# Kernel tuning notes

Hardware: AMD Instinct MI355X
Metric: run time of the kernel (lower is better)

The kernel has to match this reference:

```python
import jax, jax.numpy as jnp
import numpy as np

B, DIM, HEADS, HW = 32, 384, 8, 48
CH = DIM // HEADS  # 48 channels per head


def pool_matrix(H, s):
    # PyTorch AdaptiveAvgPool2d binning: start=floor(i*H/s), end=ceil((i+1)*H/s)
    P = np.zeros((s, H), np.float32)
    for i in range(s):
        a = (i * H) // s
        b = -((-(i + 1) * H) // s)
        P[i, a:b] = 1.0 / (b - a)
    return jnp.asarray(P)


def dwconv(x, w, b, p):
    # depthwise conv, NCHW, kernel [C,1,k,k], stride 1, symmetric pad p
    y = jax.lax.conv_general_dilated(
        x, w, (1, 1), [(p, p), (p, p)],
        dimension_numbers=('NCHW', 'OIHW', 'NCHW'),
        feature_group_count=x.shape[1])
    if b is not None:
        y = y + b[None, :, None, None]
    return y


def setup_inputs() -> dict:
    key = jax.random.key(0)
    ks = jax.random.split(key, 10)
    s = 0.02
    return {
        'x': jax.random.normal(ks[0], (B, DIM, HW, HW), jnp.float32),
        'ln_w': jnp.ones((DIM,), jnp.float32),
        'ln_b': jnp.zeros((DIM,), jnp.float32),
        'w_qkv': jax.random.normal(ks[1], (3 * DIM, DIM), jnp.float32) * s,
        'w_dw': jax.random.normal(ks[2], (3 * DIM, 1, 3, 3), jnp.float32) * s,
        'temperature': jnp.ones((HEADS, 1, 1), jnp.float32),
        'conv3_w': jax.random.normal(ks[3], (3 * CH, 1, 3, 3), jnp.float32) * s,
        'conv3_b': jnp.zeros((3 * CH,), jnp.float32),
        'conv5_w': jax.random.normal(ks[4], (3 * CH, 1, 5, 5), jnp.float32) * s,
        'conv5_b': jnp.zeros((3 * CH,), jnp.float32),
        'conv7_w': jax.random.normal(ks[5], (2 * CH, 1, 7, 7), jnp.float32) * s,
        'conv7_b': jnp.zeros((2 * CH,), jnp.float32),
        'w_proj': jax.random.normal(ks[6], (DIM, DIM), jnp.float32) * s,
    }


def reference(x, ln_w, ln_b, w_qkv, w_dw, temperature,
              conv3_w, conv3_b, conv5_w, conv5_b, conv7_w, conv7_b, w_proj):
    b, C, H, W = x.shape
    heads, Ch = HEADS, C // HEADS
    N = H * W
    # WithBias LayerNorm over channel dim (biased variance, eps 1e-5)
    mu = x.mean(axis=1, keepdims=True)
    var = ((x - mu) ** 2).mean(axis=1, keepdims=True)
    xn = (x - mu) / jnp.sqrt(var + 1e-5) * ln_w[None, :, None, None] + ln_b[None, :, None, None]
    # qkv: 1x1 conv then depthwise 3x3 (groups = 3*dim)
    qkv = jnp.einsum('bchw,oc->bohw', xn, w_qkv)
    qkv = dwconv(qkv, w_dw, None, 1)
    q, k, v = jnp.split(qkv, 3, axis=1)
    q = q.reshape(b, heads, Ch, N)
    k = k.reshape(b, heads, Ch, N)
    v = v.reshape(b, heads, Ch, N)
    # L2-normalize along token dim (F.normalize eps=1e-12)
    qn = q / jnp.maximum(jnp.linalg.norm(q, axis=-1, keepdims=True), 1e-12)
    kn = k / jnp.maximum(jnp.linalg.norm(k, axis=-1, keepdims=True), 1e-12)
    # channel attention [b,h,Ch,Ch]
    attn = jax.nn.relu(jnp.einsum('bhcn,bhdn->bhcd', qn, kn) * temperature[None])
    # ---- FilterModule (crpe) ----
    v_img = v.reshape(b, heads * Ch, H, W)
    # low-pass: 4 equal channel chunks, adaptive avg pool to (1,3,5,7), bilinear up
    chunk = (heads * Ch) // 4
    lp_parts = []
    for idx, sz in enumerate((1, 3, 5, 7)):
        part = v_img[:, idx * chunk:(idx + 1) * chunk]
        Pr = pool_matrix(H, sz)
        Pc = pool_matrix(W, sz)
        pooled = jnp.einsum('ph,bchw,qw->bcpq', Pr, part, Pc)
        lp_parts.append(jax.image.resize(pooled, (b, chunk, H, W), method='linear'))
    LP = jax.nn.relu(jnp.concatenate(lp_parts, axis=1))
    # high-pass: grouped depthwise convs on [3Ch, 3Ch, 2Ch] channel splits
    s0, s1 = 3 * Ch, 3 * Ch
    HP = jnp.concatenate([
        dwconv(v_img[:, :s0], conv3_w, conv3_b, 1),
        dwconv(v_img[:, s0:s0 + s1], conv5_w, conv5_b, 2),
        dwconv(v_img[:, s0 + s1:], conv7_w, conv7_b, 3),
    ], axis=1)
    HP = HP.reshape(b, heads, Ch, N)
    LPf = LP.reshape(b, heads, Ch, N)
    crpe = qn * HP + LPf
    # ---- output ----
    out = jnp.einsum('bhcd,bhdn->bhcn', attn, v)
    out = (Ch ** -0.5) * out + crpe
    out = out.reshape(b, C, H, W)
    out = jnp.einsum('bchw,oc->bohw', out, w_proj)
    return out
```

## Files before the change

### kernel.cpp

```cpp
#include <hip/hip_runtime.h>

typedef unsigned short u16;
typedef short sh4 __attribute__((ext_vector_type(4)));
typedef short short8 __attribute__((ext_vector_type(8)));
typedef u16 ush8 __attribute__((ext_vector_type(8)));
typedef __bf16 bf16x8 __attribute__((ext_vector_type(8)));
typedef float f32x4 __attribute__((ext_vector_type(4)));

#define NB 32
#define CDIM 384
#define NSP 2304
#define QCH 1152

__device__ __forceinline__ float b2f(u16 u) {
    union { unsigned i; float f; } v; v.i = ((unsigned)u) << 16; return v.f;
}
__device__ __forceinline__ u16 f2b(float f) {
    union { float f; unsigned i; } v; v.f = f;
    unsigned r = v.i + 0x7FFFu + ((v.i >> 16) & 1u);
    return (u16)(r >> 16);
}
__device__ __forceinline__ void gload16(const u16* g, u16* l) {
    __builtin_amdgcn_global_load_lds((const __attribute__((address_space(1))) unsigned int*)(g),
                                     (__attribute__((address_space(3))) unsigned int*)(l), 16, 0, 0);
}

__global__ __launch_bounds__(256) void k_prep(const float* __restrict__ wqkv,
                                              const float* __restrict__ wproj,
                                              u16* __restrict__ wqkv_bf,
                                              u16* __restrict__ wproj_bf) {
    int i = blockIdx.x * 256 + threadIdx.x;
    if (i < QCH * CDIM) wqkv_bf[i] = f2b(wqkv[i]);
    if (i < CDIM * CDIM) wproj_bf[i] = f2b(wproj[i]);
}

__global__ __launch_bounds__(256) void k_ln(const float* __restrict__ x,
                                            const float* __restrict__ lnw,
                                            const float* __restrict__ lnb,
                                            u16* __restrict__ xnt) {
    __shared__ float s_sum[4][64], s_sq[4][64], s_mu[64], s_rs[64];
    __shared__ u16 s_tile[64][392];
    int b = blockIdx.y, n0 = blockIdx.x * 64;
    int tid = threadIdx.x, c4 = tid >> 6, nl = tid & 63;
    int cbase = c4 * 96;
    const float* xb = x + (size_t)b * CDIM * NSP + (size_t)cbase * NSP + n0 + nl;
    float v[96];
    float sum = 0.f, sq = 0.f;
#pragma unroll
    for (int j = 0; j < 96; j++) {
        v[j] = xb[(size_t)j * NSP];
        sum += v[j]; sq += v[j] * v[j];
    }
    s_sum[c4][nl] = sum; s_sq[c4][nl] = sq;
    __syncthreads();
    if (tid < 64) {
        float s = s_sum[0][tid] + s_sum[1][tid] + s_sum[2][tid] + s_sum[3][tid];
        float q = s_sq[0][tid] + s_sq[1][tid] + s_sq[2][tid] + s_sq[3][tid];
        float mu = s * (1.f / CDIM);
        float var = q * (1.f / CDIM) - mu * mu;
        s_mu[tid] = mu; s_rs[tid] = rsqrtf(var + 1e-5f);
    }
    __syncthreads();
    float mu = s_mu[nl], rs = s_rs[nl];
#pragma unroll
    for (int j = 0; j < 96; j++) {
        int c = cbase + j;
        s_tile[nl][c] = f2b((v[j] - mu) * rs * lnw[c] + lnb[c]);
    }
    __syncthreads();
    u16* o = xnt + ((size_t)b * NSP + n0) * CDIM;
    for (int i = tid; i < 64 * 48; i += 256) {
        int row = i / 48, c8 = i % 48;
        *(short8*)(o + row * CDIM + c8 * 8) = *(const short8*)(&s_tile[row][c8 * 8]);
    }
}

__global__ __launch_bounds__(256) void k_gemm(const u16* __restrict__ A,
                                              const u16* __restrict__ Bt,
                                              void* __restrict__ Cmat, int M, int f32out) {
    __shared__ __align__(16) u16 As[128 * 64];
    __shared__ __align__(16) u16 Bs[128 * 64];
    int tid = threadIdx.x;
    int bxn = blockIdx.x, bym = blockIdx.y, bz = blockIdx.z;
    int wave = tid >> 6, lane = tid & 63, wr = wave >> 1, wc = wave & 1;
    int lr = lane & 15, lk = lane >> 4;
    f32x4 acc[4][4];
#pragma unroll
    for (int m = 0; m < 4; m++)
#pragma unroll
        for (int n = 0; n < 4; n++) acc[m][n] = (f32x4){0.f, 0.f, 0.f, 0.f};
    int coloff = ((lane & 7) ^ (lane >> 3)) * 8;
    int rsub = lane >> 3;
    const u16* Ag = A + (size_t)(bym * 128 + wave * 32 + rsub) * 384 + coloff;
    const u16* Bg = Bt + ((size_t)bz * NSP + bxn * 128 + wave * 32 + rsub) * 384 + coloff;
    u16* Al = As + (wave * 4) * 512;
    u16* Bl = Bs + (wave * 4) * 512;
    for (int k0 = 0; k0 < 384; k0 += 64) {
#pragma unroll
        for (int i = 0; i < 4; i++) {
            gload16(Ag + (size_t)(i * 8) * 384 + k0, Al + i * 512);
            gload16(Bg + (size_t)(i * 8) * 384 + k0, Bl + i * 512);
        }
        __syncthreads();
        short8 bfr[4][2];
#pragma unroll
        for (int n = 0; n < 4; n++) {
            int row = wc * 64 + n * 16 + lr;
#pragma unroll
            for (int h = 0; h < 2; h++)
                bfr[n][h] = *(const short8*)(Bs + row * 64 + ((h * 4 + lk) ^ (lr & 7)) * 8);
        }
#pragma unroll
        for (int m = 0; m < 4; m++) {
            int row = wr * 64 + m * 16 + lr;
            short8 a0 = *(const short8*)(As + row * 64 + ((lk) ^ (lr & 7)) * 8);
            short8 a1 = *(const short8*)(As + row * 64 + ((4 + lk) ^ (lr & 7)) * 8);
#pragma unroll
            for (int n = 0; n < 4; n++) {
                acc[m][n] = __builtin_amdgcn_mfma_f32_16x16x32_bf16(
                    __builtin_bit_cast(bf16x8, a0), __builtin_bit_cast(bf16x8, bfr[n][0]),
                    acc[m][n], 0, 0, 0);
                acc[m][n] = __builtin_amdgcn_mfma_f32_16x16x32_bf16(
                    __builtin_bit_cast(bf16x8, a1), __builtin_bit_cast(bf16x8, bfr[n][1]),
                    acc[m][n], 0, 0, 0);
            }
        }
        __syncthreads();
    }
#pragma unroll
    for (int m = 0; m < 4; m++)
#pragma unroll
        for (int n = 0; n < 4; n++) {
            int row = bym * 128 + wr * 64 + m * 16 + lk * 4;
            int col = bxn * 128 + wc * 64 + n * 16 + lr;
            if (f32out) {
                float* cp = (float*)Cmat + ((size_t)bz * M + row) * NSP + col;
#pragma unroll
                for (int r = 0; r < 4; r++) cp[(size_t)r * NSP] = acc[m][n][r];
            } else {
                u16* cp = (u16*)Cmat + ((size_t)bz * M + row) * NSP + col;
#pragma unroll
                for (int r = 0; r < 4; r++) cp[(size_t)r * NSP] = f2b(acc[m][n][r]);
            }
        }
}

__global__ __launch_bounds__(192) void k_dw3(u16* __restrict__ qkv,
                                             const float* __restrict__ wdw,
                                             float* __restrict__ sumsq) {
    __shared__ u16 s_in[4 * 2304];
    __shared__ float s_part[192];
    int bx = blockIdx.x, b = blockIdx.y, tid = threadIdx.x;
    u16* gbase = qkv + ((size_t)b * QCH + bx * 4) * NSP;
#pragma unroll
    for (int i = 0; i < 6; i++) {
        int c = tid + i * 192;
        *(ush8*)(&s_in[c * 8]) = *(const ush8*)(gbase + c * 8);
    }
    int p = tid / 48, y = tid % 48;
    int ch = bx * 4 + p;
    float w[9];
#pragma unroll
    for (int i = 0; i < 9; i++) w[i] = wdw[ch * 9 + i];
    __syncthreads();
    const u16* L = &s_in[p * 2304];
    ush8 r0[6], r1[6], r2[6];
#pragma unroll
    for (int o = 0; o < 6; o++) {
        r1[o] = *(const ush8*)(L + y * 48 + o * 8);
        if (y > 0)  r0[o] = *(const ush8*)(L + (y - 1) * 48 + o * 8); else r0[o] = 0;
        if (y < 47) r2[o] = *(const ush8*)(L + (y + 1) * 48 + o * 8); else r2[o] = 0;
    }
    float ss = 0.f;
    short8 outv[6];
#pragma unroll
    for (int g = 0; g < 6; g++) {
        float a0[10], a1[10], a2[10];
#pragma unroll
        for (int j = 0; j < 10; j++) {
            int xi = g * 8 - 1 + j;
            if (xi < 0 || xi >= 48) { a0[j] = 0.f; a1[j] = 0.f; a2[j] = 0.f; }
            else {
                a0[j] = b2f(r0[xi >> 3][xi & 7]);
                a1[j] = b2f(r1[xi >> 3][xi & 7]);
                a2[j] = b2f(r2[xi >> 3][xi & 7]);
            }
        }
        union { u16 u[8]; short8 v; } pk;
#pragma unroll
        for (int x = 0; x < 8; x++) {
            float o = a0[x] * w[0] + a0[x + 1] * w[1] + a0[x + 2] * w[2]
                    + a1[x] * w[3] + a1[x + 1] * w[4] + a1[x + 2] * w[5]
                    + a2[x] * w[6] + a2[x + 1] * w[7] + a2[x + 2] * w[8];
            ss += o * o;
            pk.u[x] = f2b(o);
        }
        outv[g] = pk.v;
    }
    s_part[tid] = ss;
    __syncthreads();
#pragma unroll
    for (int g = 0; g < 6; g++)
        *(short8*)(&s_in[p * 2304 + y * 48 + g * 8]) = outv[g];
    __syncthreads();
#pragma unroll
    for (int i = 0; i < 6; i++) {
        int c = tid + i * 192;
        *(ush8*)(gbase + c * 8) = *(const ush8*)(&s_in[c * 8]);
    }
    if (bx < 192 && tid < 4) {
        float s = 0.f;
        for (int i = 0; i < 48; i++) s += s_part[tid * 48 + i];
        sumsq[b * 768 + bx * 4 + tid] = s;
    }
}

__global__ __launch_bounds__(512) void k_attn(const u16* __restrict__ qkv,
                                              const float* __restrict__ sumsq,
                                              const float* __restrict__ temp,
                                              u16* __restrict__ attn) {
    __shared__ float s_part[8][48 * 48];
    int h = blockIdx.x, b = blockIdx.y, tid = threadIdx.x;
    int wave = tid >> 6, lane = tid & 63;
    int lr = lane & 15, lk = lane >> 4;
    const u16* qp = qkv + ((size_t)b * QCH + h * 48) * NSP;
    const u16* kp = qkv + ((size_t)b * QCH + 384 + h * 48) * NSP;
    f32x4 acc[3][3];
#pragma unroll
    for (int m = 0; m < 3; m++)
#pragma unroll
        for (int n = 0; n < 3; n++) acc[m][n] = (f32x4){0.f, 0.f, 0.f, 0.f};
    int k0 = wave * 288 + lk * 8;
    short8 af[3], bf[3], afn[3], bfn[3];
#pragma unroll
    for (int m = 0; m < 3; m++) {
        af[m] = *(const short8*)(qp + (size_t)(m * 16 + lr) * NSP + k0);
        bf[m] = *(const short8*)(kp + (size_t)(m * 16 + lr) * NSP + k0);
    }
    for (int s = 0; s < 9; s++) {
        if (s < 8) {
#pragma unroll
            for (int m = 0; m < 3; m++) {
                afn[m] = *(const short8*)(qp + (size_t)(m * 16 + lr) * NSP + k0 + 32 * (s + 1));
                bfn[m] = *(const short8*)(kp + (size_t)(m * 16 + lr) * NSP + k0 + 32 * (s + 1));
            }
        }
#pragma unroll
        for (int m = 0; m < 3; m++)
#pragma unroll
            for (int n = 0; n < 3; n++)
                acc[m][n] = __builtin_amdgcn_mfma_f32_16x16x32_bf16(
                    __builtin_bit_cast(bf16x8, af[m]), __builtin_bit_cast(bf16x8, bf[n]),
                    acc[m][n], 0, 0, 0);
#pragma unroll
        for (int m = 0; m < 3; m++) { af[m] = afn[m]; bf[m] = bfn[m]; }
    }
#pragma unroll
    for (int m = 0; m < 3; m++)
#pragma unroll
        for (int n = 0; n < 3; n++)
#pragma unroll
            for (int r = 0; r < 4; r++)
                s_part[wave][(m * 16 + lk * 4 + r) * 48 + n * 16 + lr] = acc[m][n][r];
    __syncthreads();
    float th = temp[h];
    const float* sqv = sumsq + b * 768 + h * 48;
    const float* skv = sumsq + b * 768 + 384 + h * 48;
    u16* ap = attn + ((size_t)(b * 8 + h)) * NSP;
    for (int f = tid; f < 2304; f += 512) {
        int c = f / 48, d = f % 48;
        float v = 0.f;
#pragma unroll
        for (int wv = 0; wv < 8; wv++) v += s_part[wv][f];
        float rq = 1.f / fmaxf(sqrtf(sqv[c]), 1e-12f);
        float rk = 1.f / fmaxf(sqrtf(skv[d]), 1e-12f);
        v *= th * rq * rk;
        ap[f] = f2b(fmaxf(v, 0.f));
    }
}

template<int KS, int CH0, int NCH>
__device__ __forceinline__ void hp_body(int g, const u16* __restrict__ qkv,
                                        const float* __restrict__ wk,
                                        const float* __restrict__ bk,
                                        u16* __restrict__ hp) {
    constexpr int PAD = KS / 2;
    constexpr int NIN = 8 + 2 * PAD;
    int t = g * 256 + threadIdx.x;
    int y = t % 48;
    int rem = t / 48;
    int chl = rem % NCH;
    int b = rem / NCH;
    int ch = CH0 + chl;
    const u16* src = qkv + ((size_t)b * QCH + 768 + ch) * NSP;
    float bias = bk[chl];
    float acc[48];
#pragma unroll
    for (int i = 0; i < 48; i++) acc[i] = bias;
    for (int dy = 0; dy < KS; dy++) {
        int yy = y - PAD + dy;
        if (yy < 0 || yy >= 48) continue;
        ush8 r[6];
#pragma unroll
        for (int o = 0; o < 6; o++) r[o] = *(const ush8*)(src + yy * 48 + o * 8);
        float wr[KS];
#pragma unroll
        for (int dx = 0; dx < KS; dx++) wr[dx] = wk[chl * KS * KS + dy * KS + dx];
#pragma unroll
        for (int g2 = 0; g2 < 6; g2++) {
            float a[NIN];
#pragma unroll
            for (int j = 0; j < NIN; j++) {
                int xi = g2 * 8 - PAD + j;
                a[j] = (xi < 0 || xi >= 48) ? 0.f : b2f(r[xi >> 3][xi & 7]);
            }
#pragma unroll
            for (int x = 0; x < 8; x++) {
                float s = 0.f;
#pragma unroll
                for (int dx = 0; dx < KS; dx++) s += a[x + dx] * wr[dx];
                acc[g2 * 8 + x] += s;
            }
        }
    }
    u16* dst = hp + ((size_t)b * CDIM + ch) * NSP + y * 48;
#pragma unroll
    for (int g2 = 0; g2 < 6; g2++) {
        union { u16 u[8]; short8 v; } pk;
#pragma unroll
        for (int x = 0; x < 8; x++) pk.u[x] = f2b(acc[g2 * 8 + x]);
        *(short8*)(dst + g2 * 8) = pk.v;
    }
}

__global__ __launch_bounds__(256) void k_hp(const u16* __restrict__ qkv,
                                            const float* __restrict__ w3, const float* __restrict__ b3,
                                            const float* __restrict__ w5, const float* __restrict__ b5,
                                            const float* __restrict__ w7, const float* __restrict__ b7,
                                            u16* __restrict__ hp) {
    int g = blockIdx.x;
    if (g < 864)       hp_body<3, 0, 144>(g, qkv, w3, b3, hp);
    else if (g < 1728) hp_body<5, 144, 144>(g - 864, qkv, w5, b5, hp);
    else               hp_body<7, 288, 96>(g - 1728, qkv, w7, b7, hp);
}

__global__ __launch_bounds__(64) void k_pool(const u16* __restrict__ qkv,
                                             float* __restrict__ pooled) {
    int c = blockIdx.x, b = blockIdx.y, tid = threadIdx.x;
    int s = 2 * (c / 96) + 1;
    __shared__ u16 s_p[2304];
    __shared__ float rp[48][7];
    const u16* src = qkv + ((size_t)b * QCH + 768 + c) * NSP;
    for (int f = tid; f < 288; f += 64)
        *(ush8*)(&s_p[f * 8]) = *(const ush8*)(src + f * 8);
    __syncthreads();
    if (tid < 48) {
        for (int q = 0; q < s; q++) {
            int a = q * 48 / s, e = ((q + 1) * 48 + s - 1) / s;
            float sum = 0.f;
            for (int xx = a; xx < e; xx++) sum += b2f(s_p[tid * 48 + xx]);
            rp[tid][q] = sum / (float)(e - a);
        }
    }
    __syncthreads();
    if (tid < s * s) {
        int p = tid / s, q = tid % s;
        int a = p * 48 / s, e = ((p + 1) * 48 + s - 1) / s;
        float sum = 0.f;
        for (int r = a; r < e; r++) sum += rp[r][q];
        pooled[((size_t)b * CDIM + c) * 49 + tid] = sum / (float)(e - a);
    }
}

__global__ __launch_bounds__(256) void k_out(const u16* __restrict__ qkv,
                                             const u16* __restrict__ attn,
                                             const float* __restrict__ sumsq,
                                             const u16* __restrict__ hp,
                                             const float* __restrict__ pooled,
                                             u16* __restrict__ tmpt) {
    int nc = blockIdx.x, h = blockIdx.y, b = blockIdx.z, tid = threadIdx.x;
    __shared__ u16 s_at[48 * 72];
    __shared__ u16 s_vt[64 * 72];
    __shared__ u16 s_q[48 * 72];
    __shared__ u16 s_hp[48 * 72];
    __shared__ float s_pool[48 * 49];
    __shared__ float s_rq[48];
    int n0 = nc * 64;
    int s = 2 * (h / 2) + 1, ss2 = s * s;
    for (int f = tid; f < 432; f += 256) *(ush8*)(&s_at[f * 8]) = (ush8)0;
    for (int f = tid; f < 576; f += 256) *(ush8*)(&s_vt[f * 8]) = (ush8)0;
    __syncthreads();
    const u16* ag = attn + ((size_t)(b * 8 + h)) * NSP;
    for (int f = tid; f < 288; f += 256) {
        int c = f / 6, j = f % 6;
        *(ush8*)(&s_at[c * 72 + j * 8]) = *(const ush8*)(ag + c * 48 + j * 8);
    }
    const u16* vsrc = qkv + ((size_t)b * QCH + 768 + h * 48) * NSP + n0;
    for (int f = tid; f < 3072; f += 256) {
        int d = f >> 6, nn = f & 63;
        s_vt[nn * 72 + d] = vsrc[(size_t)d * NSP + nn];
    }
    const u16* qsrc = qkv + ((size_t)b * QCH + h * 48) * NSP + n0;
    const u16* hsrc = hp + ((size_t)b * CDIM + h * 48) * NSP + n0;
    for (int f = tid; f < 384; f += 256) {
        int d = f >> 3, nn8 = (f & 7) * 8;
        *(ush8*)(&s_q[d * 72 + nn8])  = *(const ush8*)(qsrc + (size_t)d * NSP + nn8);
        *(ush8*)(&s_hp[d * 72 + nn8]) = *(const ush8*)(hsrc + (size_t)d * NSP + nn8);
    }
    const float* psrc = pooled + ((size_t)b * CDIM + h * 48) * 49;
    for (int f = tid; f < 48 * ss2; f += 256) {
        int c = f / ss2, idx = f - c * ss2;
        s_pool[c * 49 + idx] = psrc[c * 49 + idx];
    }
    if (tid < 48) {
        float sq_ = sumsq[b * 768 + h * 48 + tid];
        s_rq[tid] = 1.f / fmaxf(sqrtf(sq_), 1e-12f);
    }
    __syncthreads();
    int wave = tid >> 6, lane = tid & 63, lr = lane & 15, lk = lane >> 4;
    f32x4 acc[3];
#pragma unroll
    for (int m = 0; m < 3; m++) acc[m] = (f32x4){0.f, 0.f, 0.f, 0.f};
#pragma unroll
    for (int ks = 0; ks < 2; ks++) {
        short8 bfr = *(const short8*)(&s_vt[(wave * 16 + lr) * 72 + ks * 32 + lk * 8]);
#pragma unroll
        for (int m = 0; m < 3; m++) {
            short8 af = *(const short8*)(&s_at[(m * 16 + lr) * 72 + ks * 32 + lk * 8]);
            acc[m] = __builtin_amdgcn_mfma_f32_16x16x32_bf16(
                __builtin_bit_cast(bf16x8, af), __builtin_bit_cast(bf16x8, bfr),
                acc[m], 0, 0, 0);
        }
    }
    const float inv = 0.14433756729740643f;
    int nl_e = wave * 16 + lr;
    int n = n0 + nl_e;
    int y = n / 48, xx = n % 48;
    int iy0 = 0, iy1 = 0, ix0 = 0, ix1 = 0;
    float fy = 0.f, fx = 0.f;
    if (s > 1) {
        float syf = (y + 0.5f) * s * (1.f / 48.f) - 0.5f;
        iy0 = (int)floorf(syf); fy = syf - (float)iy0;
        iy1 = min(iy0 + 1, s - 1); iy0 = max(iy0, 0);
        float sxf = (xx + 0.5f) * s * (1.f / 48.f) - 0.5f;
        ix0 = (int)floorf(sxf); fx = sxf - (float)ix0;
        ix1 = min(ix0 + 1, s - 1); ix0 = max(ix0, 0);
    }
    u16* tp = tmpt + ((size_t)b * NSP + n) * CDIM + h * 48;
#pragma unroll
    for (int m = 0; m < 3; m++) {
        int cb = m * 16 + lk * 4;
        union { u16 u[4]; sh4 v; } pk;
#pragma unroll
        for (int r = 0; r < 4; r++) {
            int ch = cb + r;
            float qv = b2f(s_q[ch * 72 + nl_e]);
            float hv = b2f(s_hp[ch * 72 + nl_e]);
            const float* P = &s_pool[ch * 49];
            float lp;
            if (s == 1) lp = P[0];
            else lp = (1.f - fy) * ((1.f - fx) * P[iy0 * s + ix0] + fx * P[iy0 * s + ix1])
                    + fy * ((1.f - fx) * P[iy1 * s + ix0] + fx * P[iy1 * s + ix1]);
            lp = fmaxf(lp, 0.f);
            pk.u[r] = f2b(inv * acc[m][r] + qv * s_rq[ch] * hv + lp);
        }
        *(sh4*)(tp + cb) = pk.v;
    }
}

extern "C" void kernel_launch(void* const* d_in, const int* in_sizes, int n_in,
                              void* d_out, int out_size, void* d_ws, size_t ws_size,
                              hipStream_t stream) {
    const float* x    = (const float*)d_in[0];
    const float* lnw  = (const float*)d_in[1];
    const float* lnb  = (const float*)d_in[2];
    const float* wqkv = (const float*)d_in[3];
    const float* wdw  = (const float*)d_in[4];
    const float* temp = (const float*)d_in[5];
    const float* w3   = (const float*)d_in[6];
    const float* b3   = (const float*)d_in[7];
    const float* w5   = (const float*)d_in[8];
    const float* b5   = (const float*)d_in[9];
    const float* w7   = (const float*)d_in[10];
    const float* b7   = (const float*)d_in[11];
    const float* wproj= (const float*)d_in[12];
    float* out = (float*)d_out;

    char* w = (char*)d_ws;
    const size_t SZ_XNT = (size_t)NB * NSP * CDIM * 2;
    const size_t SZ_QKV = (size_t)NB * QCH * NSP * 2;
    u16* xnt      = (u16*)w;
    u16* qkvb     = (u16*)(w + SZ_XNT);
    u16* hpb      = (u16*)(w + SZ_XNT + SZ_QKV);
    char* tail    = w + SZ_XNT + SZ_QKV + (size_t)NB * CDIM * NSP * 2;
    float* sumsq  = (float*)tail;
    u16*  attnb   = (u16*)(sumsq + NB * 768);
    float* pooled = (float*)(attnb + (size_t)NB * 8 * NSP);
    u16* wqkv_bf  = (u16*)(pooled + (size_t)NB * CDIM * 49);
    u16* wproj_bf = wqkv_bf + (size_t)QCH * CDIM;
    u16* tmpt = xnt;

    k_prep <<<dim3((QCH * CDIM + 255) / 256), 256, 0, stream>>>(wqkv, wproj, wqkv_bf, wproj_bf);
    k_ln   <<<dim3(36, NB), 256, 0, stream>>>(x, lnw, lnb, xnt);
    k_gemm <<<dim3(18, 9, NB), 256, 0, stream>>>(wqkv_bf, xnt, qkvb, QCH, 0);
    k_dw3  <<<dim3(288, NB), 192, 0, stream>>>(qkvb, wdw, sumsq);
    k_attn <<<dim3(8, NB), 512, 0, stream>>>(qkvb, sumsq, temp, attnb);
    k_hp   <<<dim3(2304), 256, 0, stream>>>(qkvb, w3, b3, w5, b5, w7, b7, hpb);
    k_pool <<<dim3(CDIM, NB), 64, 0, stream>>>(qkvb, pooled);
    k_out  <<<dim3(36, 8, NB), 256, 0, stream>>>(qkvb, attnb, sumsq, hpb, pooled, tmpt);
    k_gemm <<<dim3(18, 3, NB), 256, 0, stream>>>(wproj_bf, tmpt, out, CDIM, 1);
}
```

Before: 442.0 us.

## Persist k_out blocks over nine spatial tiles and read q/hp directly

k_out now launches 4 blocks per (head, batch) instead of 36. Each block loops over 9 tiles of 64 positions, loading the attention matrix, pooled values and norms once and keeping the attention A-fragments in registers. Only the padding columns of the shared tiles are zeroed, and q and hp are read straight from global memory instead of being staged in shared memory. This cuts redundant per-block setup and shared-memory traffic. The cost is fewer blocks (1024) for latency hiding, and strided per-element global loads for q and hp.

Result: faster. 425.0 us (-3.8%).

```diff
diff --git a/kernel.cpp b/kernel.cpp
--- a/kernel.cpp
+++ b/kernel.cpp
@@ -378,93 +378,102 @@
                                              const u16* __restrict__ hp,
                                              const float* __restrict__ pooled,
                                              u16* __restrict__ tmpt) {
-    int nc = blockIdx.x, h = blockIdx.y, b = blockIdx.z, tid = threadIdx.x;
-    __shared__ u16 s_at[48 * 72];
-    __shared__ u16 s_vt[64 * 72];
-    __shared__ u16 s_q[48 * 72];
-    __shared__ u16 s_hp[48 * 72];
+    int ncg = blockIdx.x, h = blockIdx.y, b = blockIdx.z, tid = threadIdx.x;
+    __shared__ __align__(16) u16 s_at[48 * 72];
+    __shared__ __align__(16) u16 s_vt[64 * 72];
     __shared__ float s_pool[48 * 49];
     __shared__ float s_rq[48];
-    int n0 = nc * 64;
     int s = 2 * (h / 2) + 1, ss2 = s * s;
-    for (int f = tid; f < 432; f += 256) *(ush8*)(&s_at[f * 8]) = (ush8)0;
-    for (int f = tid; f < 576; f += 256) *(ush8*)(&s_vt[f * 8]) = (ush8)0;
-    __syncthreads();
+    if (tid < 96) {
+        int c = tid >> 1, col8 = 48 + (tid & 1) * 8;
+        *(ush8*)(&s_at[c * 72 + col8]) = (ush8)0;
+    }
+    if (tid < 128) {
+        int nn = tid >> 1, col8 = 48 + (tid & 1) * 8;
+        *(ush8*)(&s_vt[nn * 72 + col8]) = (ush8)0;
+    }
     const u16* ag = attn + ((size_t)(b * 8 + h)) * NSP;
     for (int f = tid; f < 288; f += 256) {
         int c = f / 6, j = f % 6;
         *(ush8*)(&s_at[c * 72 + j * 8]) = *(const ush8*)(ag + c * 48 + j * 8);
     }
-    const u16* vsrc = qkv + ((size_t)b * QCH + 768 + h * 48) * NSP + n0;
-    for (int f = tid; f < 3072; f += 256) {
-        int d = f >> 6, nn = f & 63;
-        s_vt[nn * 72 + d] = vsrc[(size_t)d * NSP + nn];
-    }
-    const u16* qsrc = qkv + ((size_t)b * QCH + h * 48) * NSP + n0;
-    const u16* hsrc = hp + ((size_t)b * CDIM + h * 48) * NSP + n0;
-    for (int f = tid; f < 384; f += 256) {
-        int d = f >> 3, nn8 = (f & 7) * 8;
-        *(ush8*)(&s_q[d * 72 + nn8])  = *(const ush8*)(qsrc + (size_t)d * NSP + nn8);
-        *(ush8*)(&s_hp[d * 72 + nn8]) = *(const ush8*)(hsrc + (size_t)d * NSP + nn8);
-    }
     const float* psrc = pooled + ((size_t)b * CDIM + h * 48) * 49;
     for (int f = tid; f < 48 * ss2; f += 256) {
         int c = f / ss2, idx = f - c * ss2;
         s_pool[c * 49 + idx] = psrc[c * 49 + idx];
     }
-    if (tid < 48) {
-        float sq_ = sumsq[b * 768 + h * 48 + tid];
-        s_rq[tid] = 1.f / fmaxf(sqrtf(sq_), 1e-12f);
-    }
-    __syncthreads();
+    if (tid < 48) s_rq[tid] = 1.f / fmaxf(sqrtf(sumsq[b * 768 + h * 48 + tid]), 1e-12f);
+
     int wave = tid >> 6, lane = tid & 63, lr = lane & 15, lk = lane >> 4;
-    f32x4 acc[3];
-#pragma unroll
-    for (int m = 0; m < 3; m++) acc[m] = (f32x4){0.f, 0.f, 0.f, 0.f};
-#pragma unroll
-    for (int ks = 0; ks < 2; ks++) {
-        short8 bfr = *(const short8*)(&s_vt[(wave * 16 + lr) * 72 + ks * 32 + lk * 8]);
+    const u16* vbase = qkv + ((size_t)b * QCH + 768 + h * 48) * NSP;
+    const u16* qbase = qkv + ((size_t)b * QCH + h * 48) * NSP;
+    const u16* hbase = hp + ((size_t)b * CDIM + h * 48) * NSP;
+    const float inv = 0.14433756729740643f;
+    short8 afr[3][2];
+
+    for (int it = 0; it < 9; it++) {
+        int n0 = (ncg * 9 + it) * 64;
+        for (int f = tid; f < 3072; f += 256) {
+            int d = f >> 6, nn = f & 63;
+            s_vt[nn * 72 + d] = vbase[(size_t)d * NSP + n0 + nn];
+        }
+        __syncthreads();
+        if (it == 0) {
+#pragma unroll
+            for (int m = 0; m < 3; m++)
+#pragma unroll
+                for (int ks = 0; ks < 2; ks++)
+                    afr[m][ks] = *(const short8*)(&s_at[(m * 16 + lr) * 72 + ks * 32 + lk * 8]);
+        }
+        short8 b0 = *(const short8*)(&s_vt[(wave * 16 + lr) * 72 + lk * 8]);
+        short8 b1 = *(const short8*)(&s_vt[(wave * 16 + lr) * 72 + 32 + lk * 8]);
+        f32x4 acc[3];
 #pragma unroll
         for (int m = 0; m < 3; m++) {
-            short8 af = *(const short8*)(&s_at[(m * 16 + lr) * 72 + ks * 32 + lk * 8]);
+            acc[m] = (f32x4){0.f, 0.f, 0.f, 0.f};
             acc[m] = __builtin_amdgcn_mfma_f32_16x16x32_bf16(
-                __builtin_bit_cast(bf16x8, af), __builtin_bit_cast(bf16x8, bfr),
+                __builtin_bit_cast(bf16x8, afr[m][0]), __builtin_bit_cast(bf16x8, b0),
                 acc[m], 0, 0, 0);
-        }
-    }
-    const float inv = 0.14433756729740643f;
-    int nl_e = wave * 16 + lr;
-    int n = n0 + nl_e;
-    int y = n / 48, xx = n % 48;
-    int iy0 = 0, iy1 = 0, ix0 = 0, ix1 = 0;
-    float fy = 0.f, fx = 0.f;
-    if (s > 1) {
-        float syf = (y + 0.5f) * s * (1.f / 48.f) - 0.5f;
-        iy0 = (int)floorf(syf); fy = syf - (float)iy0;
-        iy1 = min(iy0 + 1, s - 1); iy0 = max(iy0, 0);
-        float sxf = (xx + 0.5f) * s * (1.f / 48.f) - 0.5f;
-        ix0 = (int)floorf(sxf); fx = sxf - (float)ix0;
-        ix1 = min(ix0 + 1, s - 1); ix0 = max(ix0, 0);
-    }
-    u16* tp = tmpt + ((size_t)b * NSP + n) * CDIM + h * 48;
-#pragma unroll
-    for (int m = 0; m < 3; m++) {
-        int cb = m * 16 + lk * 4;
-        union { u16 u[4]; sh4 v; } pk;
-#pragma unroll
-        for (int r = 0; r < 4; r++) {
-            int ch = cb + r;
-            float qv = b2f(s_q[ch * 72 + nl_e]);
-            float hv = b2f(s_hp[ch * 72 + nl_e]);
-            const float* P = &s_pool[ch * 49];
-            float lp;
-            if (s == 1) lp = P[0];
-            else lp = (1.f - fy) * ((1.f - fx) * P[iy0 * s + ix0] + fx * P[iy0 * s + ix1])
-                    + fy * ((1.f - fx) * P[iy1 * s + ix0] + fx * P[iy1 * s + ix1]);
-            lp = fmaxf(lp, 0.f);
-            pk.u[r] = f2b(inv * acc[m][r] + qv * s_rq[ch] * hv + lp);
-        }
-        *(sh4*)(tp + cb) = pk.v;
+            acc[m] = __builtin_amdgcn_mfma_f32_16x16x32_bf16(
+                __builtin_bit_cast(bf16x8, afr[m][1]), __builtin_bit_cast(bf16x8, b1),
+                acc[m], 0, 0, 0);
+        }
+        int nl_e = wave * 16 + lr;
+        int n = n0 + nl_e;
+        int y = n / 48, xx = n % 48;
+        int iy0 = 0, iy1 = 0, ix0 = 0, ix1 = 0;
+        float fy = 0.f, fx = 0.f;
+        if (s > 1) {
+            float syf = (y + 0.5f) * s * (1.f / 48.f) - 0.5f;
+            iy0 = (int)floorf(syf); fy = syf - (float)iy0;
+            iy1 = min(iy0 + 1, s - 1); iy0 = max(iy0, 0);
+            float sxf = (xx + 0.5f) * s * (1.f / 48.f) - 0.5f;
+            ix0 = (int)floorf(sxf); fx = sxf - (float)ix0;
+            ix1 = min(ix0 + 1, s - 1); ix0 = max(ix0, 0);
+        }
+        const u16* qp = qbase + n;
+        const u16* hq = hbase + n;
+        u16* tp = tmpt + ((size_t)b * NSP + n) * CDIM + h * 48;
+#pragma unroll
+        for (int m = 0; m < 3; m++) {
+            int cb = m * 16 + lk * 4;
+            union { u16 u[4]; sh4 v; } pk;
+#pragma unroll
+            for (int r = 0; r < 4; r++) {
+                int ch = cb + r;
+                float qv = b2f(qp[(size_t)ch * NSP]);
+                float hv = b2f(hq[(size_t)ch * NSP]);
+                const float* P = &s_pool[ch * 49];
+                float lp;
+                if (s == 1) lp = P[0];
+                else lp = (1.f - fy) * ((1.f - fx) * P[iy0 * s + ix0] + fx * P[iy0 * s + ix1])
+                        + fy * ((1.f - fx) * P[iy1 * s + ix0] + fx * P[iy1 * s + ix1]);
+                lp = fmaxf(lp, 0.f);
+                pk.u[r] = f2b(inv * acc[m][r] + qv * s_rq[ch] * hv + lp);
+            }
+            *(sh4*)(tp + cb) = pk.v;
+        }
+        __syncthreads();
     }
 }
 
@@ -507,6 +516,6 @@
     k_attn <<<dim3(8, NB), 512, 0, stream>>>(qkvb, sumsq, temp, attnb);
     k_hp   <<<dim3(2304), 256, 0, stream>>>(qkvb, w3, b3, w5, b5, w7, b7, hpb);
     k_pool <<<dim3(CDIM, NB), 64, 0, stream>>>(qkvb, pooled);
-    k_out  <<<dim3(36, 8, NB), 256, 0, stream>>>(qkvb, attnb, sumsq, hpb, pooled, tmpt);
+    k_out  <<<dim3(4, 8, NB), 256, 0, stream>>>(qkvb, attnb, sumsq, hpb, pooled, tmpt);
     k_gemm <<<dim3(18, 3, NB), 256, 0, stream>>>(wproj_bf, tmpt, out, CDIM, 1);
 }
```
